# Optimization experiments

Hardware: AMD Instinct MI355X
Metric: run time of the kernel (lower is better)

Reference implementation:

```python
import jax, jax.numpy as jnp
import numpy as np
import math

NUM_HEADS = 16
HEAD_DIM = 64
NUM_BUCKETS = 256
MAX_DISTANCE = 16384
ROPE_BASE = 10000.0


def _rel_pos_bucket(rel):
    # faithful to RelativePositionEncoding._relative_position_bucket
    ab = jnp.abs(rel)
    max_exact = NUM_BUCKETS // 4  # 64
    half = NUM_BUCKETS // 2       # 128
    is_small = ab < max_exact
    safe = jnp.maximum(ab, 1).astype(jnp.float32)
    large = max_exact + (jnp.log(safe / max_exact) / math.log(MAX_DISTANCE / max_exact) * (half - max_exact)).astype(jnp.int32)
    large = jnp.minimum(large, half - 1)
    bucket = jnp.where(is_small, ab, large)
    bucket = jnp.where(rel < 0, half + bucket, bucket)
    return bucket


def _rope_cos_sin(seq_len):
    # RotaryPositionEncoding with rope dim = 2*head_dim: num_features = head_dim,
    # inv_freq over arange(0, head_dim, 2)/head_dim, interleaved repeat to head_dim
    inv_freq = 1.0 / (ROPE_BASE ** (jnp.arange(0, HEAD_DIM, 2, dtype=jnp.float32) / HEAD_DIM))
    pos = jnp.arange(seq_len, dtype=jnp.float32)
    freqs = pos[:, None] * inv_freq[None, :]          # [S, HEAD_DIM//2]
    cos = jnp.repeat(jnp.cos(freqs), 2, axis=-1)      # [S, HEAD_DIM]
    sin = jnp.repeat(jnp.sin(freqs), 2, axis=-1)
    return cos, sin


def _rotate_half(t):
    h = t.shape[-1] // 2
    return jnp.concatenate([-t[..., h:], t[..., :h]], axis=-1)


def setup_inputs() -> dict:
    key = jax.random.key(0)
    ks = jax.random.split(key, 6)
    B, S, E = 2, 2048, 1024
    x = jax.random.normal(ks[0], (B, S, E), dtype=jnp.float32)
    Wq = jax.random.normal(ks[1], (E, E), dtype=jnp.float32) * 0.02
    Wk = jax.random.normal(ks[2], (E, E), dtype=jnp.float32) * 0.02
    Wv = jax.random.normal(ks[3], (E, E), dtype=jnp.float32) * 0.02
    Wo = jax.random.normal(ks[4], (E, E), dtype=jnp.float32) * 0.02
    rel_emb = jax.random.normal(ks[5], (NUM_BUCKETS, NUM_HEADS, HEAD_DIM), dtype=jnp.float32) * 0.02
    return {"x": x, "Wq": Wq, "Wk": Wk, "Wv": Wv, "Wo": Wo, "rel_emb": rel_emb}


def reference(x, Wq, Wk, Wv, Wo, rel_emb):
    B, S, E = x.shape
    H, D = NUM_HEADS, HEAD_DIM

    def split_heads(t):
        return t.reshape(B, S, H, D).transpose(0, 2, 1, 3)  # [B,H,S,D]

    q = split_heads(x @ Wq)
    k = split_heads(x @ Wk)
    v = split_heads(x @ Wv)

    # inline RoPE on q/k (cos/sin broadcast over batch & heads)
    cos, sin = _rope_cos_sin(S)  # [S, D]
    q = q * cos + _rotate_half(q) * sin
    k = k * cos + _rotate_half(k) * sin

    # relative-position bucket bias: q . rel_emb[bucket(i-j)]
    pos = jnp.arange(S)
    bucket = _rel_pos_bucket(pos[:, None] - pos[None, :])      # [S, S]
    q_rel = jnp.einsum('bhqd,nhd->bhqn', q, rel_emb)           # [B,H,S,NUM_BUCKETS]
    bias = jnp.take_along_axis(q_rel, bucket[None, None, :, :], axis=-1)  # [B,H,S,S]

    scale = 1.0 / math.sqrt(D)
    scores = (jnp.einsum('bhqd,bhkd->bhqk', q, k) + bias) * scale

    causal = pos[:, None] >= pos[None, :]
    scores = jnp.where(causal[None, None], scores, jnp.float32(-1e9))
    attn = jax.nn.softmax(scores, axis=-1)

    out = jnp.einsum('bhqk,bhkd->bhqd', attn, v)
    out = out.transpose(0, 2, 1, 3).reshape(B, S, E)
    return out @ Wo
```

## Files before the change

### kernel.cpp

```cpp
#include <hip/hip_runtime.h>
#include <hip/hip_bf16.h>
#include <math.h>


typedef __attribute__((ext_vector_type(8))) short bf16x8;
typedef __attribute__((ext_vector_type(4))) float f32x4;

static __device__ __forceinline__ unsigned short f2bf(float x) {
    unsigned u = __float_as_uint(x);
    unsigned r = (u + 0x7fffu + ((u >> 16) & 1u)) >> 16;
    return (unsigned short)r;
}
static __device__ __forceinline__ float bf2f(unsigned short h) {
    return __uint_as_float(((unsigned)h) << 16);
}
static __device__ __forceinline__ unsigned cvtpk(float lo, float hi) {
    unsigned r;
    asm("v_cvt_pk_bf16_f32 %0, %1, %2" : "=v"(r) : "v"(lo), "v"(hi));
    return r;
}
static __device__ __forceinline__ float fexp2(float x) {
    return __builtin_amdgcn_exp2f(x);
}

#define GLOAD16(gp, lp)                                                            \
    __builtin_amdgcn_global_load_lds(                                              \
        (const __attribute__((address_space(1))) unsigned int*)(gp),               \
        (__attribute__((address_space(3))) unsigned int*)(lp), 16, 0, 0)

__global__ void prep(const float* __restrict__ x,
                     const float* __restrict__ W0, const float* __restrict__ W1,
                     const float* __restrict__ W2, const float* __restrict__ W3,
                     const float* __restrict__ rel,
                     unsigned short* __restrict__ xb,
                     unsigned short* __restrict__ T0, unsigned short* __restrict__ T1,
                     unsigned short* __restrict__ T2, unsigned short* __restrict__ T3,
                     unsigned short* __restrict__ relTb, float* __restrict__ ropeT)
{
    __shared__ unsigned short tls[64][65];
    const int id  = blockIdx.x;
    const int tid = threadIdx.x;
    if (id < 2048) {
        const size_t t = (size_t)id * 256 + tid;
        const float4* p = (const float4*)(x + t*8);
        float4 a = p[0], b = p[1];
        unsigned w0 = cvtpk(a.x, a.y), w1 = cvtpk(a.z, a.w);
        unsigned w2 = cvtpk(b.x, b.y), w3 = cvtpk(b.z, b.w);
        *(uint4*)(xb + t*8) = make_uint4(w0, w1, w2, w3);
    } else if (id < 3072) {
        const int local = id - 2048;
        const int z  = local >> 8;
        const float* W = (z == 0) ? W0 : (z == 1) ? W1 : (z == 2) ? W2 : W3;
        unsigned short* Wt = (z == 0) ? T0 : (z == 1) ? T1 : (z == 2) ? T2 : T3;
        const int bb  = local & 255;
        const int bxt = bb & 15;
        const int byt = bb >> 4;
        const int r   = tid >> 2;
        const int c0  = (tid & 3) * 16;
        const float* src = W + (size_t)(byt*64 + r)*1024 + bxt*64 + c0;
#pragma unroll
        for (int j = 0; j < 4; ++j) {
            float4 vv = ((const float4*)src)[j];
            tls[c0 + j*4 + 0][r] = f2bf(vv.x);
            tls[c0 + j*4 + 1][r] = f2bf(vv.y);
            tls[c0 + j*4 + 2][r] = f2bf(vv.z);
            tls[c0 + j*4 + 3][r] = f2bf(vv.w);
        }
        __syncthreads();
        unsigned short* dst = Wt + (size_t)(bxt*64 + r)*1024 + byt*64 + c0;
        unsigned w[8];
#pragma unroll
        for (int j = 0; j < 8; ++j)
            w[j] = (unsigned)tls[r][c0 + 2*j] | ((unsigned)tls[r][c0 + 2*j + 1] << 16);
        *(uint4*)(dst)     = make_uint4(w[0], w[1], w[2], w[3]);
        *(uint4*)(dst + 8) = make_uint4(w[4], w[5], w[6], w[7]);
    } else if (id < 3136) {
        const int t  = (id - 3072) * 256 + tid;
        const int d0 = (t & 7) * 8;
        const int n  = (t >> 3) & 127;
        const int h  = t >> 10;
        const float* src = rel + ((size_t)(n*16 + h))*64 + d0;
        float4 a = ((const float4*)src)[0], b = ((const float4*)src)[1];
        unsigned w0 = cvtpk(a.x, a.y), w1 = cvtpk(a.z, a.w);
        unsigned w2 = cvtpk(b.x, b.y), w3 = cvtpk(b.z, b.w);
        *(uint4*)(relTb + (size_t)h*8192 + n*64 + d0) = make_uint4(w0, w1, w2, w3);
    } else {
        const int idx = (id - 3136) * 256 + tid;
        const int s = idx >> 4, f = idx & 15;
        const float CC = 0.41524101186092029f;
        const float if0 = exp2f(-(float)f * CC);
        const float if1 = exp2f(-(float)(f + 16) * CC);
        const float a0 = (float)s * if0;
        const float a1 = (float)s * if1;
        *(float4*)(ropeT + (size_t)idx*4) =
            make_float4(__cosf(a0), __sinf(a0), __cosf(a1), __sinf(a1));
    }
}

#define GEMM_STAGE(t, buf)                                                             \
    {                                                                                  \
        const int k0s = (t) * 64;                                                      \
        _Pragma("unroll")                                                              \
        for (int j = 0; j < 4; ++j) {                                                  \
            GLOAD16(agp + (size_t)(j*32 + srow)*1024 + k0s, &Als[buf][0] + j*2048 + tid*8); \
            GLOAD16(bgp + (size_t)(j*32 + srow)*1024 + k0s, &Bls[buf][0] + j*2048 + tid*8); \
        }                                                                              \
    }

#define GEMM_COMPUTE(buf)                                                              \
    {                                                                                  \
        _Pragma("unroll")                                                              \
        for (int ks = 0; ks < 2; ++ks) {                                               \
            bf16x8 af[4], bfr[4];                                                      \
            _Pragma("unroll")                                                          \
            for (int m = 0; m < 4; ++m)                                                \
                af[m] = *(const bf16x8*)&Als[buf][(wr + m*16 + (lane & 15))*64 + ks*32 + (lane >> 4)*8]; \
            _Pragma("unroll")                                                          \
            for (int n = 0; n < 4; ++n)                                                \
                bfr[n] = *(const bf16x8*)&Bls[buf][(wc + n*16 + (lane & 15))*64 + ks*32 + (lane >> 4)*8]; \
            _Pragma("unroll")                                                          \
            for (int m = 0; m < 4; ++m)                                                \
                _Pragma("unroll")                                                      \
                for (int n = 0; n < 4; ++n)                                            \
                    acc[m][n] = __builtin_amdgcn_mfma_f32_16x16x32_bf16(af[m], bfr[n], acc[m][n], 0, 0, 0); \
        }                                                                              \
    }

__global__ __launch_bounds__(256) void gemm_qkv(const unsigned short* __restrict__ A,
    const unsigned short* __restrict__ wtq, const unsigned short* __restrict__ wtk,
    const unsigned short* __restrict__ wtv, const float* __restrict__ ropeT,
    unsigned short* __restrict__ qb, unsigned short* __restrict__ kbb,
    unsigned short* __restrict__ vTb)
{
    __shared__ __align__(16) unsigned short Als[2][8192];
    __shared__ __align__(16) unsigned short Bls[2][8192];
    const int z = blockIdx.z;
    const unsigned short* Bt = (z == 0) ? wtq : (z == 1) ? wtk : wtv;

    const int tid  = threadIdx.x;
    const int wave = tid >> 6, lane = tid & 63;
    const int wr = (wave >> 1) * 64, wc = (wave & 1) * 64;
    const int bx = blockIdx.x, by = blockIdx.y;
    const int srow = tid >> 3;
    const unsigned short* agp = A  + (size_t)(by*128)*1024 + (tid & 7)*8;
    const unsigned short* bgp = Bt + (size_t)(bx*128)*1024 + (tid & 7)*8;

    f32x4 acc[4][4];
#pragma unroll
    for (int m = 0; m < 4; ++m)
#pragma unroll
        for (int n = 0; n < 4; ++n) acc[m][n] = (f32x4)0.f;

    GEMM_STAGE(0, 0);
    __syncthreads();
    int cur = 0;
    for (int t = 0; t < 16; ++t) {
        if (t < 15) GEMM_STAGE(t + 1, cur ^ 1);
        GEMM_COMPUTE(cur);
        __syncthreads();
        cur ^= 1;
    }

    if (z == 2) {
#pragma unroll
        for (int m = 0; m < 4; ++m) {
            const int r0 = by*128 + wr + m*16 + (lane >> 4)*4;
#pragma unroll
            for (int n = 0; n < 4; ++n) {
                const int col = bx*128 + wc + n*16 + (lane & 15);
                const int bb = r0 >> 11, ss = r0 & 2047;
                const int hh = col >> 6, dd = col & 63;
                unsigned r01 = cvtpk(acc[m][n][0], acc[m][n][1]);
                unsigned r23 = cvtpk(acc[m][n][2], acc[m][n][3]);
                *(uint2*)(vTb + (((size_t)bb*16 + hh)*64 + dd)*2048 + ss) = make_uint2(r01, r23);
            }
        }
    } else {
        unsigned short* O = z ? kbb : qb;
        const float qscl = z ? 1.0f : 0.1803368801111204f;
#pragma unroll
        for (int n = 0; n < 2; ++n) {
            const int dd = n*16 + (lane & 15);
            const int f  = dd >> 1;
            const int col = bx*128 + wc + n*16 + (lane & 15);
            const int hh = col >> 6;
#pragma unroll
            for (int m = 0; m < 4; ++m) {
                const int r0 = by*128 + wr + m*16 + (lane >> 4)*4;
#pragma unroll
                for (int rg = 0; rg < 4; ++rg) {
                    const int row = r0 + rg;
                    const int bb = row >> 11, s = row & 2047;
                    const float4 cs = *(const float4*)(ropeT + ((size_t)(s*16 + f))*4);
                    const float x0 = acc[m][n][rg];
                    const float x1 = acc[m][n + 2][rg];
                    const float o0 = (x0 * cs.x - x1 * cs.y) * qscl;
                    const float o1 = (x1 * cs.z + x0 * cs.w) * qscl;
                    unsigned short* ob = O + (((size_t)bb*16 + hh)*2048 + s)*64 + dd;
                    ob[0]  = f2bf(o0);
                    ob[32] = f2bf(o1);
                }
            }
        }
    }
}

__global__ __launch_bounds__(256) void gemm_o(const unsigned short* __restrict__ A,
                                              const unsigned short* __restrict__ Bt,
                                              float* __restrict__ C)
{
    __shared__ __align__(16) unsigned short Als[2][8192];
    __shared__ __align__(16) unsigned short Bls[2][8192];
    const int tid  = threadIdx.x;
    const int wave = tid >> 6, lane = tid & 63;
    const int wr = (wave >> 1) * 64, wc = (wave & 1) * 64;
    const int bx = blockIdx.x, by = blockIdx.y;
    const int srow = tid >> 3;
    const unsigned short* agp = A  + (size_t)(by*128)*1024 + (tid & 7)*8;
    const unsigned short* bgp = Bt + (size_t)(bx*128)*1024 + (tid & 7)*8;

    f32x4 acc[4][4];
#pragma unroll
    for (int m = 0; m < 4; ++m)
#pragma unroll
        for (int n = 0; n < 4; ++n) acc[m][n] = (f32x4)0.f;

    GEMM_STAGE(0, 0);
    __syncthreads();
    int cur = 0;
    for (int t = 0; t < 16; ++t) {
        if (t < 15) GEMM_STAGE(t + 1, cur ^ 1);
        GEMM_COMPUTE(cur);
        __syncthreads();
        cur ^= 1;
    }

#pragma unroll
    for (int m = 0; m < 4; ++m) {
        const int r0 = by*128 + wr + m*16 + (lane >> 4)*4;
#pragma unroll
        for (int n = 0; n < 4; ++n) {
            const int col = bx*128 + wc + n*16 + (lane & 15);
#pragma unroll
            for (int rg = 0; rg < 4; ++rg)
                C[(size_t)(r0 + rg)*1024 + col] = acc[m][n][rg];
        }
    }
}

__global__ __launch_bounds__(256) void qrel_mfma(const unsigned short* __restrict__ qb,
                                                 const unsigned short* __restrict__ relTb,
                                                 unsigned short* __restrict__ qrelb)
{
    __shared__ __align__(16) unsigned short Rls[8192];
    __shared__ __align__(16) unsigned short Qls[8192];
    const int tid  = threadIdx.x;
    const int wave = tid >> 6, lane = tid & 63;
    const int wr = (wave >> 1) * 64;
    const int wc = (wave & 1) * 64;
    const int s0 = blockIdx.x * 128;
    const int bh = blockIdx.y;
    const int h  = bh & 15;

    const unsigned short* qsrc = qb + ((size_t)bh*2048 + s0)*64;
    const unsigned short* rsrc = relTb + (size_t)h*8192;
#pragma unroll
    for (int j = 0; j < 4; ++j) {
        GLOAD16(rsrc + j*2048 + tid*8, &Rls[0] + j*2048 + tid*8);
        GLOAD16(qsrc + j*2048 + tid*8, &Qls[0] + j*2048 + tid*8);
    }

    f32x4 acc[4][4];
#pragma unroll
    for (int m = 0; m < 4; ++m)
#pragma unroll
        for (int n = 0; n < 4; ++n) acc[m][n] = (f32x4)0.f;

    __syncthreads();

#pragma unroll
    for (int ks = 0; ks < 2; ++ks) {
        bf16x8 rf[4], qf[4];
#pragma unroll
        for (int m = 0; m < 4; ++m)
            rf[m] = *(const bf16x8*)&Rls[(wr + m*16 + (lane & 15))*64 + ks*32 + (lane >> 4)*8];
#pragma unroll
        for (int n = 0; n < 4; ++n)
            qf[n] = *(const bf16x8*)&Qls[(wc + n*16 + (lane & 15))*64 + ks*32 + (lane >> 4)*8];
#pragma unroll
        for (int m = 0; m < 4; ++m)
#pragma unroll
            for (int n = 0; n < 4; ++n)
                acc[m][n] = __builtin_amdgcn_mfma_f32_16x16x32_bf16(rf[m], qf[n], acc[m][n], 0, 0, 0);
    }

#pragma unroll
    for (int m = 0; m < 4; ++m) {
        const int bkt0 = wr + m*16 + (lane >> 4)*4;
#pragma unroll
        for (int n = 0; n < 4; ++n) {
            const int srow = s0 + wc + n*16 + (lane & 15);
            unsigned r01 = cvtpk(acc[m][n][0], acc[m][n][1]);
            unsigned r23 = cvtpk(acc[m][n][2], acc[m][n][3]);
            *(uint2*)(qrelb + ((size_t)bh*2048 + srow)*128 + bkt0) = make_uint2(r01, r23);
        }
    }
}

__global__ __launch_bounds__(512) void flash_mfma(
    const unsigned short* __restrict__ qb, const unsigned short* __restrict__ kb,
    const unsigned short* __restrict__ vT, const unsigned short* __restrict__ qrelb,
    unsigned short* __restrict__ ctxb)
{
    __shared__ __align__(16) unsigned short kls[2][4096];
    __shared__ __align__(16) unsigned short vtls[2][4096];
    __shared__ __align__(16) unsigned short qrels[128*138];

    const int tid = threadIdx.x;
    const int id  = blockIdx.x;
    const int bh  = id & 31;
    const int px  = 15 - (id >> 5);
    const int i0  = px * 128;

    const int w   = tid >> 6;
    const int l   = tid & 63;
    const int q15 = l & 15;
    const int g   = l >> 4;
    const int iq  = i0 + w*16 + q15;
    const int tdiag  = 2*px + (w >> 2);
    const int ntiles = 2*px + 2;

    const size_t headoff = (size_t)bh * 2048 * 64;
    const int half = tid >> 8;
    const int t8   = tid & 255;
    const unsigned short* gbase = half ? (vT + headoff) : (kb + headoff);
    const int jstride = half ? 1 : 64;
    int soff[2], doff[2];
#pragma unroll
    for (int i = 0; i < 2; ++i) {
        const int D = t8*16 + i*4096;
        const int r = D >> 7, c = (D >> 4) & 7;
        soff[i] = half ? (r*2048 + ((c ^ (r & 7))*8)) : (r*64 + ((c ^ (r & 7))*8));
        doff[i] = D;
    }

    for (int idx = tid; idx < 2048; idx += 512) {
        const int r = idx >> 4, c8 = idx & 15;
        uint4 vv = *(const uint4*)(qrelb + ((size_t)bh*2048 + i0 + r)*128 + c8*8);
        unsigned* d = (unsigned*)&qrels[r*138 + c8*8];
        d[0] = vv.x; d[1] = vv.y; d[2] = vv.z; d[3] = vv.w;
    }
    {
        char* lb = half ? (char*)vtls[0] : (char*)kls[0];
#pragma unroll
        for (int i = 0; i < 2; ++i) GLOAD16(gbase + soff[i], lb + doff[i]);
    }

    bf16x8 qf0, qf1;
    {
        const unsigned short* qrow = qb + ((size_t)bh*2048 + iq)*64;
        qf0 = *(const bf16x8*)(qrow + g*8);
        qf1 = *(const bf16x8*)(qrow + 32 + g*8);
    }

    f32x4 acc[4];
#pragma unroll
    for (int d = 0; d < 4; ++d) acc[d] = (f32x4)0.f;
    float mrun = -INFINITY, lsum = 0.f;

    const int qrow_lds = (w*16 + q15) * 138;
    const int srcA = ((2*g) & 3)*16 + q15;
    const int srcB = ((2*g + 1) & 3)*16 + q15;

    __syncthreads();

    int cur = 0;
    for (int t = 0; t < ntiles; ++t) {
        const int j0 = t * 64;
        if (t + 1 < ntiles) {
            const unsigned short* gt = gbase + (size_t)(j0 + 64) * jstride;
            char* lb = half ? (char*)vtls[cur ^ 1] : (char*)kls[cur ^ 1];
#pragma unroll
            for (int i = 0; i < 2; ++i) GLOAD16(gt + soff[i], lb + doff[i]);
        }

        if (t <= tdiag) {
            __builtin_amdgcn_s_setprio(1);
            f32x4 s[4];
#pragma unroll
            for (int ss = 0; ss < 4; ++ss) s[ss] = (f32x4)0.f;
#pragma unroll
            for (int ks = 0; ks < 2; ++ks) {
                const bf16x8 qq = ks ? qf1 : qf0;
                const int gr = ((ks*4 + g) ^ (q15 & 7)) * 8;
#pragma unroll
                for (int ss = 0; ss < 4; ++ss) {
                    bf16x8 kf = *(const bf16x8*)&kls[cur][(ss*16 + q15)*64 + gr];
                    s[ss] = __builtin_amdgcn_mfma_f32_16x16x32_bf16(kf, qq, s[ss], 0, 0, 0);
                }
            }

            const int relbase = iq - j0 - g*4;
            float sv[16];
            float tmax = -INFINITY;
            if (t != tdiag) {
#pragma unroll
                for (int ss = 0; ss < 4; ++ss) {
#pragma unroll
                    for (int r = 0; r < 4; ++r) {
                        const int bi = relbase - ss*16 - r;
                        int bkt;
                        if (bi < 64) bkt = bi;
                        else {
                            bkt = 64 + (int)(__log2f((float)bi) * 8.0f - 48.0f);
                            bkt = bkt > 127 ? 127 : bkt;
                        }
                        const float bias = bf2f(qrels[qrow_lds + bkt]);
                        const float val = s[ss][r] + bias;
                        sv[ss*4 + r] = val;
                        tmax = fmaxf(tmax, val);
                    }
                }
            } else {
#pragma unroll
                for (int ss = 0; ss < 4; ++ss) {
#pragma unroll
                    for (int r = 0; r < 4; ++r) {
                        const int rel = relbase - ss*16 - r;
                        const int bi = rel < 0 ? 0 : rel;
                        int bkt;
                        if (bi < 64) bkt = bi;
                        else {
                            bkt = 64 + (int)(__log2f((float)bi) * 8.0f - 48.0f);
                            bkt = bkt > 127 ? 127 : bkt;
                        }
                        const float bias = bf2f(qrels[qrow_lds + bkt]);
                        float val = s[ss][r] + bias;
                        val = (rel >= 0) ? val : -1e30f;
                        sv[ss*4 + r] = val;
                        tmax = fmaxf(tmax, val);
                    }
                }
            }
            tmax = fmaxf(tmax, __shfl_xor(tmax, 16));
            tmax = fmaxf(tmax, __shfl_xor(tmax, 32));

            float newm = mrun;
            if (!__all(tmax - mrun <= 8.0f)) {
                newm = fmaxf(mrun, tmax);
                const float corr = fexp2(mrun - newm);
                lsum *= corr;
#pragma unroll
                for (int d = 0; d < 4; ++d) {
                    acc[d][0] *= corr; acc[d][1] *= corr; acc[d][2] *= corr; acc[d][3] *= corr;
                }
                mrun = newm;
            }

            float p[16], ps = 0.f;
#pragma unroll
            for (int j = 0; j < 16; ++j) { p[j] = fexp2(sv[j] - newm); ps += p[j]; }
            ps += __shfl_xor(ps, 16);
            ps += __shfl_xor(ps, 32);
            lsum += ps;

#pragma unroll
            for (int ck = 0; ck < 2; ++ck) {
                unsigned w00 = cvtpk(p[8*ck+0], p[8*ck+1]);
                unsigned w01 = cvtpk(p[8*ck+2], p[8*ck+3]);
                unsigned w10 = cvtpk(p[8*ck+4], p[8*ck+5]);
                unsigned w11 = cvtpk(p[8*ck+6], p[8*ck+7]);
                unsigned a0 = (unsigned)__shfl((int)w00, srcA);
                unsigned b0 = (unsigned)__shfl((int)w10, srcA);
                unsigned a1 = (unsigned)__shfl((int)w01, srcA);
                unsigned b1 = (unsigned)__shfl((int)w11, srcA);
                unsigned a2 = (unsigned)__shfl((int)w00, srcB);
                unsigned b2 = (unsigned)__shfl((int)w10, srcB);
                unsigned a3 = (unsigned)__shfl((int)w01, srcB);
                unsigned b3 = (unsigned)__shfl((int)w11, srcB);
                union { unsigned u[4]; bf16x8 v; } pu;
                pu.u[0] = (g < 2) ? a0 : b0;
                pu.u[1] = (g < 2) ? a1 : b1;
                pu.u[2] = (g < 2) ? a2 : b2;
                pu.u[3] = (g < 2) ? a3 : b3;
#pragma unroll
                for (int dblk = 0; dblk < 4; ++dblk) {
                    const int d2 = dblk*16 + q15;
                    bf16x8 vf = *(const bf16x8*)&vtls[cur][d2*64 + (((ck*4 + g) ^ (d2 & 7))*8)];
                    acc[dblk] = __builtin_amdgcn_mfma_f32_16x16x32_bf16(vf, pu.v, acc[dblk], 0, 0, 0);
                }
            }
            __builtin_amdgcn_s_setprio(0);
        }

        __syncthreads();
        cur ^= 1;
    }

    const float inv = 1.0f / lsum;
    const int s2 = iq;
    const int b2 = bh >> 4, hh = bh & 15;
    unsigned short* obase = ctxb + (((size_t)b2*2048 + s2)*16 + hh)*64;
#pragma unroll
    for (int dblk = 0; dblk < 4; ++dblk) {
        const int d0 = dblk*16 + g*4;
        unsigned r01 = cvtpk(acc[dblk][0]*inv, acc[dblk][1]*inv);
        unsigned r23 = cvtpk(acc[dblk][2]*inv, acc[dblk][3]*inv);
        *(uint2*)(obase + d0) = make_uint2(r01, r23);
    }
}

extern "C" void kernel_launch(void* const* d_in, const int* in_sizes, int n_in,
                              void* d_out, int out_size, void* d_ws, size_t ws_size,
                              hipStream_t stream)
{
    const float* x   = (const float*)d_in[0];
    const float* Wq  = (const float*)d_in[1];
    const float* Wk  = (const float*)d_in[2];
    const float* Wv  = (const float*)d_in[3];
    const float* Wo  = (const float*)d_in[4];
    const float* rel = (const float*)d_in[5];

    float* ws = (float*)d_ws;
    unsigned short* qb    = (unsigned short*)(ws + 8388608);
    unsigned short* kbb   = (unsigned short*)(ws + 10485760);
    unsigned short* qrelb = (unsigned short*)(ws + 12582912);
    unsigned short* vTb   = (unsigned short*)(ws + 16777216);
    unsigned short* xb    = (unsigned short*)(ws + 18874368);
    unsigned short* wtq   = (unsigned short*)(ws + 20971520);
    unsigned short* wtk   = (unsigned short*)(ws + 21495808);
    unsigned short* wtv   = (unsigned short*)(ws + 22020096);
    unsigned short* wto   = (unsigned short*)(ws + 22544384);
    unsigned short* relTb = (unsigned short*)(ws + 23068672);
    float*          ropeT = ws + 23134208;
    unsigned short* ctxb  = (unsigned short*)ws;

    prep<<<3264, 256, 0, stream>>>(x, Wq, Wk, Wv, Wo, rel, xb, wtq, wtk, wtv, wto, relTb, ropeT);
    gemm_qkv<<<dim3(8, 32, 3), 256, 0, stream>>>(xb, wtq, wtk, wtv, ropeT, qb, kbb, vTb);
    qrel_mfma<<<dim3(16, 32), 256, 0, stream>>>(qb, relTb, qrelb);
    flash_mfma<<<512, 512, 0, stream>>>(qb, kbb, vTb, qrelb, ctxb);
    gemm_o<<<dim3(8, 32), 256, 0, stream>>>(ctxb, wto, (float*)d_out);
}
```

Measured before the change: 186.3 us.

## Process two 16-row query groups per wave in flash attention

```diff
diff --git a/kernel.cpp b/kernel.cpp
--- a/kernel.cpp
+++ b/kernel.cpp
@@ -307,7 +307,7 @@
     }
 }
 
-__global__ __launch_bounds__(512) void flash_mfma(
+__global__ __launch_bounds__(256) void flash_mfma(
     const unsigned short* __restrict__ qb, const unsigned short* __restrict__ kb,
     const unsigned short* __restrict__ vT, const unsigned short* __restrict__ qrelb,
     unsigned short* __restrict__ ctxb)
@@ -326,25 +326,25 @@
     const int l   = tid & 63;
     const int q15 = l & 15;
     const int g   = l >> 4;
-    const int iq  = i0 + w*16 + q15;
-    const int tdiag  = 2*px + (w >> 2);
+    const int iqA = i0 + w*32 + q15;
+    const int iqB = iqA + 16;
+    const int tdiag  = 2*px + (w >> 1);
     const int ntiles = 2*px + 2;
 
     const size_t headoff = (size_t)bh * 2048 * 64;
-    const int half = tid >> 8;
-    const int t8   = tid & 255;
+    const int half = tid >> 7;
     const unsigned short* gbase = half ? (vT + headoff) : (kb + headoff);
     const int jstride = half ? 1 : 64;
-    int soff[2], doff[2];
-#pragma unroll
-    for (int i = 0; i < 2; ++i) {
-        const int D = t8*16 + i*4096;
+    int soff[4], doff[4];
+#pragma unroll
+    for (int i = 0; i < 4; ++i) {
+        const int D = (tid & 127)*16 + i*2048;
         const int r = D >> 7, c = (D >> 4) & 7;
         soff[i] = half ? (r*2048 + ((c ^ (r & 7))*8)) : (r*64 + ((c ^ (r & 7))*8));
         doff[i] = D;
     }
 
-    for (int idx = tid; idx < 2048; idx += 512) {
+    for (int idx = tid; idx < 2048; idx += 256) {
         const int r = idx >> 4, c8 = idx & 15;
         uint4 vv = *(const uint4*)(qrelb + ((size_t)bh*2048 + i0 + r)*128 + c8*8);
         unsigned* d = (unsigned*)&qrels[r*138 + c8*8];
@@ -353,26 +353,120 @@
     {
         char* lb = half ? (char*)vtls[0] : (char*)kls[0];
 #pragma unroll
-        for (int i = 0; i < 2; ++i) GLOAD16(gbase + soff[i], lb + doff[i]);
-    }
-
-    bf16x8 qf0, qf1;
+        for (int i = 0; i < 4; ++i) GLOAD16(gbase + soff[i], lb + doff[i]);
+    }
+
+    bf16x8 qA0, qA1, qB0, qB1;
     {
-        const unsigned short* qrow = qb + ((size_t)bh*2048 + iq)*64;
-        qf0 = *(const bf16x8*)(qrow + g*8);
-        qf1 = *(const bf16x8*)(qrow + 32 + g*8);
-    }
-
-    f32x4 acc[4];
-#pragma unroll
-    for (int d = 0; d < 4; ++d) acc[d] = (f32x4)0.f;
-    float mrun = -INFINITY, lsum = 0.f;
-
-    const int qrow_lds = (w*16 + q15) * 138;
+        const unsigned short* qrowA = qb + ((size_t)bh*2048 + iqA)*64;
+        const unsigned short* qrowB = qb + ((size_t)bh*2048 + iqB)*64;
+        qA0 = *(const bf16x8*)(qrowA + g*8);
+        qA1 = *(const bf16x8*)(qrowA + 32 + g*8);
+        qB0 = *(const bf16x8*)(qrowB + g*8);
+        qB1 = *(const bf16x8*)(qrowB + 32 + g*8);
+    }
+
+    f32x4 accA[4], accB[4];
+#pragma unroll
+    for (int d = 0; d < 4; ++d) { accA[d] = (f32x4)0.f; accB[d] = (f32x4)0.f; }
+    float mrunA = -INFINITY, lsumA = 0.f;
+    float mrunB = -INFINITY, lsumB = 0.f;
+
+    const int qlA = (w*32 + q15) * 138;
+    const int qlB = (w*32 + 16 + q15) * 138;
     const int srcA = ((2*g) & 3)*16 + q15;
     const int srcB = ((2*g + 1) & 3)*16 + q15;
 
     __syncthreads();
+
+#define SOFTMAX_GROUP(sG, iqG, qlG, mrunG, lsumG, accG, pwG)                           \
+    {                                                                                  \
+        const int relbase = (iqG) - j0 - g*4;                                          \
+        float sv[16];                                                                  \
+        float tmax = -INFINITY;                                                        \
+        if (t != tdiag) {                                                              \
+            _Pragma("unroll")                                                          \
+            for (int ss = 0; ss < 4; ++ss) {                                           \
+                _Pragma("unroll")                                                      \
+                for (int r = 0; r < 4; ++r) {                                          \
+                    const int bi = relbase - ss*16 - r;                                \
+                    int bkt;                                                           \
+                    if (bi < 64) bkt = bi;                                             \
+                    else {                                                             \
+                        bkt = 64 + (int)(__log2f((float)bi) * 8.0f - 48.0f);           \
+                        bkt = bkt > 127 ? 127 : bkt;                                   \
+                    }                                                                  \
+                    const float bias = bf2f(qrels[(qlG) + bkt]);                       \
+                    const float val = sG[ss][r] + bias;                                \
+                    sv[ss*4 + r] = val;                                                \
+                    tmax = fmaxf(tmax, val);                                           \
+                }                                                                      \
+            }                                                                          \
+        } else {                                                                       \
+            _Pragma("unroll")                                                          \
+            for (int ss = 0; ss < 4; ++ss) {                                           \
+                _Pragma("unroll")                                                      \
+                for (int r = 0; r < 4; ++r) {                                          \
+                    const int rel = relbase - ss*16 - r;                               \
+                    const int bi = rel < 0 ? 0 : rel;                                  \
+                    int bkt;                                                           \
+                    if (bi < 64) bkt = bi;                                             \
+                    else {                                                             \
+                        bkt = 64 + (int)(__log2f((float)bi) * 8.0f - 48.0f);           \
+                        bkt = bkt > 127 ? 127 : bkt;                                   \
+                    }                                                                  \
+                    const float bias = bf2f(qrels[(qlG) + bkt]);                       \
+                    float val = sG[ss][r] + bias;                                      \
+                    val = (rel >= 0) ? val : -1e30f;                                   \
+                    sv[ss*4 + r] = val;                                                \
+                    tmax = fmaxf(tmax, val);                                           \
+                }                                                                      \
+            }                                                                          \
+        }                                                                              \
+        tmax = fmaxf(tmax, __shfl_xor(tmax, 16));                                      \
+        tmax = fmaxf(tmax, __shfl_xor(tmax, 32));                                      \
+        float newm = mrunG;                                                            \
+        if (!__all(tmax - mrunG <= 8.0f)) {                                            \
+            newm = fmaxf(mrunG, tmax);                                                 \
+            const float corr = fexp2(mrunG - newm);                                    \
+            lsumG *= corr;                                                             \
+            _Pragma("unroll")                                                          \
+            for (int d = 0; d < 4; ++d) {                                              \
+                accG[d][0] *= corr; accG[d][1] *= corr;                                \
+                accG[d][2] *= corr; accG[d][3] *= corr;                                \
+            }                                                                          \
+            mrunG = newm;                                                              \
+        }                                                                              \
+        float p[16], ps = 0.f;                                                         \
+        _Pragma("unroll")                                                              \
+        for (int j = 0; j < 16; ++j) { p[j] = fexp2(sv[j] - newm); ps += p[j]; }       \
+        ps += __shfl_xor(ps, 16);                                                      \
+        ps += __shfl_xor(ps, 32);                                                      \
+        lsumG += ps;                                                                   \
+        _Pragma("unroll")                                                              \
+        for (int ck = 0; ck < 2; ++ck) {                                               \
+            pwG[ck][0] = cvtpk(p[8*ck+0], p[8*ck+1]);                                  \
+            pwG[ck][1] = cvtpk(p[8*ck+2], p[8*ck+3]);                                  \
+            pwG[ck][2] = cvtpk(p[8*ck+4], p[8*ck+5]);                                  \
+            pwG[ck][3] = cvtpk(p[8*ck+6], p[8*ck+7]);                                  \
+        }                                                                              \
+    }
+
+#define BUILD_PU(pu, pwG, ck)                                                          \
+    {                                                                                  \
+        unsigned a0 = (unsigned)__shfl((int)pwG[ck][0], srcA);                         \
+        unsigned b0 = (unsigned)__shfl((int)pwG[ck][2], srcA);                         \
+        unsigned a1 = (unsigned)__shfl((int)pwG[ck][1], srcA);                         \
+        unsigned b1 = (unsigned)__shfl((int)pwG[ck][3], srcA);                         \
+        unsigned a2 = (unsigned)__shfl((int)pwG[ck][0], srcB);                         \
+        unsigned b2 = (unsigned)__shfl((int)pwG[ck][2], srcB);                         \
+        unsigned a3 = (unsigned)__shfl((int)pwG[ck][1], srcB);                         \
+        unsigned b3 = (unsigned)__shfl((int)pwG[ck][3], srcB);                         \
+        pu.u[0] = (g < 2) ? a0 : b0;                                                   \
+        pu.u[1] = (g < 2) ? a1 : b1;                                                   \
+        pu.u[2] = (g < 2) ? a2 : b2;                                                   \
+        pu.u[3] = (g < 2) ? a3 : b3;                                                   \
+    }
 
     int cur = 0;
     for (int t = 0; t < ntiles; ++t) {
@@ -381,113 +475,42 @@
             const unsigned short* gt = gbase + (size_t)(j0 + 64) * jstride;
             char* lb = half ? (char*)vtls[cur ^ 1] : (char*)kls[cur ^ 1];
 #pragma unroll
-            for (int i = 0; i < 2; ++i) GLOAD16(gt + soff[i], lb + doff[i]);
+            for (int i = 0; i < 4; ++i) GLOAD16(gt + soff[i], lb + doff[i]);
         }
 
         if (t <= tdiag) {
             __builtin_amdgcn_s_setprio(1);
-            f32x4 s[4];
-#pragma unroll
-            for (int ss = 0; ss < 4; ++ss) s[ss] = (f32x4)0.f;
+            f32x4 sA[4], sB[4];
+#pragma unroll
+            for (int ss = 0; ss < 4; ++ss) { sA[ss] = (f32x4)0.f; sB[ss] = (f32x4)0.f; }
 #pragma unroll
             for (int ks = 0; ks < 2; ++ks) {
-                const bf16x8 qq = ks ? qf1 : qf0;
+                const bf16x8 qqA = ks ? qA1 : qA0;
+                const bf16x8 qqB = ks ? qB1 : qB0;
                 const int gr = ((ks*4 + g) ^ (q15 & 7)) * 8;
 #pragma unroll
                 for (int ss = 0; ss < 4; ++ss) {
                     bf16x8 kf = *(const bf16x8*)&kls[cur][(ss*16 + q15)*64 + gr];
-                    s[ss] = __builtin_amdgcn_mfma_f32_16x16x32_bf16(kf, qq, s[ss], 0, 0, 0);
+                    sA[ss] = __builtin_amdgcn_mfma_f32_16x16x32_bf16(kf, qqA, sA[ss], 0, 0, 0);
+                    sB[ss] = __builtin_amdgcn_mfma_f32_16x16x32_bf16(kf, qqB, sB[ss], 0, 0, 0);
                 }
             }
 
-            const int relbase = iq - j0 - g*4;
-            float sv[16];
-            float tmax = -INFINITY;
-            if (t != tdiag) {
-#pragma unroll
-                for (int ss = 0; ss < 4; ++ss) {
-#pragma unroll
-                    for (int r = 0; r < 4; ++r) {
-                        const int bi = relbase - ss*16 - r;
-                        int bkt;
-                        if (bi < 64) bkt = bi;
-                        else {
-                            bkt = 64 + (int)(__log2f((float)bi) * 8.0f - 48.0f);
-                            bkt = bkt > 127 ? 127 : bkt;
-                        }
-                        const float bias = bf2f(qrels[qrow_lds + bkt]);
-                        const float val = s[ss][r] + bias;
-                        sv[ss*4 + r] = val;
-                        tmax = fmaxf(tmax, val);
-                    }
-                }
-            } else {
-#pragma unroll
-                for (int ss = 0; ss < 4; ++ss) {
-#pragma unroll
-                    for (int r = 0; r < 4; ++r) {
-                        const int rel = relbase - ss*16 - r;
-                        const int bi = rel < 0 ? 0 : rel;
-                        int bkt;
-                        if (bi < 64) bkt = bi;
-                        else {
-                            bkt = 64 + (int)(__log2f((float)bi) * 8.0f - 48.0f);
-                            bkt = bkt > 127 ? 127 : bkt;
-                        }
-                        const float bias = bf2f(qrels[qrow_lds + bkt]);
-                        float val = s[ss][r] + bias;
-                        val = (rel >= 0) ? val : -1e30f;
-                        sv[ss*4 + r] = val;
-                        tmax = fmaxf(tmax, val);
-                    }
-                }
-            }
-            tmax = fmaxf(tmax, __shfl_xor(tmax, 16));
-            tmax = fmaxf(tmax, __shfl_xor(tmax, 32));
-
-            float newm = mrun;
-            if (!__all(tmax - mrun <= 8.0f)) {
-                newm = fmaxf(mrun, tmax);
-                const float corr = fexp2(mrun - newm);
-                lsum *= corr;
-#pragma unroll
-                for (int d = 0; d < 4; ++d) {
-                    acc[d][0] *= corr; acc[d][1] *= corr; acc[d][2] *= corr; acc[d][3] *= corr;
-                }
-                mrun = newm;
-            }
-
-            float p[16], ps = 0.f;
-#pragma unroll
-            for (int j = 0; j < 16; ++j) { p[j] = fexp2(sv[j] - newm); ps += p[j]; }
-            ps += __shfl_xor(ps, 16);
-            ps += __shfl_xor(ps, 32);
-            lsum += ps;
+            unsigned pwA[2][4], pwB[2][4];
+            SOFTMAX_GROUP(sA, iqA, qlA, mrunA, lsumA, accA, pwA);
+            SOFTMAX_GROUP(sB, iqB, qlB, mrunB, lsumB, accB, pwB);
 
 #pragma unroll
             for (int ck = 0; ck < 2; ++ck) {
-                unsigned w00 = cvtpk(p[8*ck+0], p[8*ck+1]);
-                unsigned w01 = cvtpk(p[8*ck+2], p[8*ck+3]);
-                unsigned w10 = cvtpk(p[8*ck+4], p[8*ck+5]);
-                unsigned w11 = cvtpk(p[8*ck+6], p[8*ck+7]);
-                unsigned a0 = (unsigned)__shfl((int)w00, srcA);
-                unsigned b0 = (unsigned)__shfl((int)w10, srcA);
-                unsigned a1 = (unsigned)__shfl((int)w01, srcA);
-                unsigned b1 = (unsigned)__shfl((int)w11, srcA);
-                unsigned a2 = (unsigned)__shfl((int)w00, srcB);
-                unsigned b2 = (unsigned)__shfl((int)w10, srcB);
-                unsigned a3 = (unsigned)__shfl((int)w01, srcB);
-                unsigned b3 = (unsigned)__shfl((int)w11, srcB);
-                union { unsigned u[4]; bf16x8 v; } pu;
-                pu.u[0] = (g < 2) ? a0 : b0;
-                pu.u[1] = (g < 2) ? a1 : b1;
-                pu.u[2] = (g < 2) ? a2 : b2;
-                pu.u[3] = (g < 2) ? a3 : b3;
+                union { unsigned u[4]; bf16x8 v; } puA, puB;
+                BUILD_PU(puA, pwA, ck);
+                BUILD_PU(puB, pwB, ck);
 #pragma unroll
                 for (int dblk = 0; dblk < 4; ++dblk) {
                     const int d2 = dblk*16 + q15;
                     bf16x8 vf = *(const bf16x8*)&vtls[cur][d2*64 + (((ck*4 + g) ^ (d2 & 7))*8)];
-                    acc[dblk] = __builtin_amdgcn_mfma_f32_16x16x32_bf16(vf, pu.v, acc[dblk], 0, 0, 0);
+                    accA[dblk] = __builtin_amdgcn_mfma_f32_16x16x32_bf16(vf, puA.v, accA[dblk], 0, 0, 0);
+                    accB[dblk] = __builtin_amdgcn_mfma_f32_16x16x32_bf16(vf, puB.v, accB[dblk], 0, 0, 0);
                 }
             }
             __builtin_amdgcn_s_setprio(0);
@@ -497,16 +520,28 @@
         cur ^= 1;
     }
 
-    const float inv = 1.0f / lsum;
-    const int s2 = iq;
     const int b2 = bh >> 4, hh = bh & 15;
-    unsigned short* obase = ctxb + (((size_t)b2*2048 + s2)*16 + hh)*64;
-#pragma unroll
-    for (int dblk = 0; dblk < 4; ++dblk) {
-        const int d0 = dblk*16 + g*4;
-        unsigned r01 = cvtpk(acc[dblk][0]*inv, acc[dblk][1]*inv);
-        unsigned r23 = cvtpk(acc[dblk][2]*inv, acc[dblk][3]*inv);
-        *(uint2*)(obase + d0) = make_uint2(r01, r23);
+    {
+        const float inv = 1.0f / lsumA;
+        unsigned short* obase = ctxb + (((size_t)b2*2048 + iqA)*16 + hh)*64;
+#pragma unroll
+        for (int dblk = 0; dblk < 4; ++dblk) {
+            const int d0 = dblk*16 + g*4;
+            unsigned r01 = cvtpk(accA[dblk][0]*inv, accA[dblk][1]*inv);
+            unsigned r23 = cvtpk(accA[dblk][2]*inv, accA[dblk][3]*inv);
+            *(uint2*)(obase + d0) = make_uint2(r01, r23);
+        }
+    }
+    {
+        const float inv = 1.0f / lsumB;
+        unsigned short* obase = ctxb + (((size_t)b2*2048 + iqB)*16 + hh)*64;
+#pragma unroll
+        for (int dblk = 0; dblk < 4; ++dblk) {
+            const int d0 = dblk*16 + g*4;
+            unsigned r01 = cvtpk(accB[dblk][0]*inv, accB[dblk][1]*inv);
+            unsigned r23 = cvtpk(accB[dblk][2]*inv, accB[dblk][3]*inv);
+            *(uint2*)(obase + d0) = make_uint2(r01, r23);
+        }
     }
 }
 
@@ -538,6 +573,6 @@
     prep<<<3264, 256, 0, stream>>>(x, Wq, Wk, Wv, Wo, rel, xb, wtq, wtk, wtv, wto, relTb, ropeT);
     gemm_qkv<<<dim3(8, 32, 3), 256, 0, stream>>>(xb, wtq, wtk, wtv, ropeT, qb, kbb, vTb);
     qrel_mfma<<<dim3(16, 32), 256, 0, stream>>>(qb, relTb, qrelb);
-    flash_mfma<<<512, 512, 0, stream>>>(qb, kbb, vTb, qrelb, ctxb);
+    flash_mfma<<<512, 256, 0, stream>>>(qb, kbb, vTb, qrelb, ctxb);
     gemm_o<<<dim3(8, 32), 256, 0, stream>>>(ctxb, wto, (float*)d_out);
 }
```

Result: slower. 203.1 us (+9.0%).
